# Kernel tuning notes

Measured on AMD Instinct MI355X. Metric: run time of the kernel, lower is better.

## Reference

```python
import jax, jax.numpy as jnp
import numpy as np

DN = ('NCHW', 'OIHW', 'NCHW')

def conv3x3(x, w):
    return jax.lax.conv_general_dilated(x, w, (1, 1), ((1, 1), (1, 1)), dimension_numbers=DN)

def dsc(x, w1, w2):
    # DynamicSparseConv: per-sample per-channel softmax 3x3 depthwise kernel + residual
    B, C, H, W = x.shape
    pooled = x.mean(axis=(2, 3))                                  # [B, C] (AdaptiveAvgPool2d(1))
    h = jax.nn.gelu(pooled @ w1.T, approximate=False)             # [B, Cr] (1x1 conv == matmul)
    logits = (h @ w2.T).reshape(B, C, 9)                          # [B, C, 9]
    wk = jax.nn.softmax(logits, axis=2)
    # 3x3 patches: [B, C*9, H, W], feature dim ordered (C, kh, kw)
    patches = jax.lax.conv_general_dilated_patches(x, (3, 3), (1, 1), ((1, 1), (1, 1)))
    patches = patches.reshape(B, C, 9, H, W)
    out = jnp.einsum('bckhw,bck->bchw', patches, wk)
    return out + x

def pixel_shuffle(x, r):
    B, C, H, W = x.shape
    c = C // (r * r)
    return x.reshape(B, c, r, r, H, W).transpose(0, 1, 4, 2, 5, 3).reshape(B, c, H * r, W * r)

def setup_inputs() -> dict:
    key = jax.random.key(0)
    ks = jax.random.split(key, 12)
    B, C, H, W, OUT = 16, 128, 64, 64, 64
    CR = max(4, C // 8)            # 16
    RE = max(4, OUT // 8)          # 8
    s = 0.05
    return {
        'x1': jax.random.normal(ks[0], (B, C, H, W), jnp.float32),
        'x2': jax.random.normal(ks[1], (B, C, H, W), jnp.float32),
        'd1_w1': jax.random.normal(ks[2], (CR, C), jnp.float32) * s,
        'd1_w2': jax.random.normal(ks[3], (9 * C, CR), jnp.float32) * s,
        'd2_w1': jax.random.normal(ks[4], (CR, C), jnp.float32) * s,
        'd2_w2': jax.random.normal(ks[5], (9 * C, CR), jnp.float32) * s,
        'align_w': jax.random.normal(ks[6], (C, 2 * C), jnp.float32) * s,
        'up_w1': jax.random.normal(ks[7], (4 * C, C, 3, 3), jnp.float32) * s,
        'up_w2': jax.random.normal(ks[8], (OUT, C), jnp.float32) * s,
        're_w1': jax.random.normal(ks[9], (RE, OUT, 3, 3), jnp.float32) * s,
        're_w2': jax.random.normal(ks[10], (OUT, RE, 3, 3), jnp.float32) * s,
    }

def reference(x1, x2, d1_w1, d1_w2, d2_w1, d2_w2, align_w, up_w1, up_w2, re_w1, re_w2):
    def dynamic_block(x):  # shared weights for both inputs (same nn.Sequential)
        x = dsc(x, d1_w1, d1_w2)
        x = jax.nn.relu(x)
        return dsc(x, d2_w1, d2_w2)
    a = dynamic_block(x1)
    b = dynamic_block(x2)
    fused = jnp.einsum('bchw,oc->bohw', jnp.concatenate([a, b], axis=1), align_w)  # 1x1 conv
    u = conv3x3(fused, up_w1)            # [B, 4C, H, W]
    u = pixel_shuffle(u, 2)              # [B, C, 2H, 2W]
    up = jnp.einsum('bchw,oc->bohw', u, up_w2)  # [B, OUT, 2H, 2W]
    re = conv3x3(jax.nn.relu(conv3x3(up, re_w1)), re_w2)
    return up + re
```

## Files before the change

### kernel.cpp

```cpp
#include <hip/hip_runtime.h>
#include <math.h>

typedef unsigned short ushort;
typedef short bf16x8 __attribute__((ext_vector_type(8)));
typedef ushort us8 __attribute__((ext_vector_type(8)));
typedef float f32x16 __attribute__((ext_vector_type(16)));
typedef float f32x4 __attribute__((ext_vector_type(4)));

static const size_t OFF_POOLED = 0;
static const size_t OFF_WK     = 4096;
static const size_t OFF_WT     = 40960;
static const size_t OFF_WF     = 188416;
static const size_t OFF_AW1    = 204800;
static const size_t OFF_AW2    = 209408;
static const size_t OFF_T      = 262144;
static const size_t OFF_AB     = 8650752;
static const size_t OFF_F      = 17039360;

static __device__ __forceinline__ ushort f2bf(float f) {
    unsigned int u = __builtin_bit_cast(unsigned int, f);
    u += 0x7FFF + ((u >> 16) & 1);
    return (ushort)(u >> 16);
}
static __device__ __forceinline__ float bf2f(ushort u) {
    return __builtin_bit_cast(float, ((unsigned int)u) << 16);
}

__global__ __launch_bounds__(256) void pool_both_kernel(const float* __restrict__ x1,
                                                        const float* __restrict__ x2,
                                                        float* __restrict__ pooled) {
    int bc = blockIdx.x;
    const float* x = (bc >> 11) ? x2 : x1;
    const float4* p = (const float4*)(x + (size_t)(bc & 2047) * 4096);
    float s = 0.f;
    for (int i = threadIdx.x; i < 1024; i += 256) {
        float4 v = p[i];
        s += v.x + v.y + v.z + v.w;
    }
    #pragma unroll
    for (int off = 32; off; off >>= 1) s += __shfl_down(s, off);
    __shared__ float r4[4];
    if ((threadIdx.x & 63) == 0) r4[threadIdx.x >> 6] = s;
    __syncthreads();
    if (threadIdx.x == 0) pooled[bc] = (r4[0] + r4[1] + r4[2] + r4[3]) * (1.f / 4096.f);
}

__global__ __launch_bounds__(128) void wk_kernel(const float* __restrict__ pooled,
                                                 const float* __restrict__ w1,
                                                 const float* __restrict__ w2,
                                                 float* __restrict__ wk) {
    int b = blockIdx.x;
    __shared__ float sp[128];
    __shared__ float sh[16];
    int t = threadIdx.x;
    sp[t] = pooled[b * 128 + t];
    __syncthreads();
    if (t < 16) {
        float acc = 0.f;
        #pragma unroll 4
        for (int c = 0; c < 128; c++) acc += w1[t * 128 + c] * sp[c];
        sh[t] = 0.5f * acc * (1.f + erff(acc * 0.70710678118654752f));
    }
    __syncthreads();
    float lg[9];
    float m = -INFINITY;
    #pragma unroll
    for (int k = 0; k < 9; k++) {
        float acc = 0.f;
        const float* wr = w2 + (size_t)(t * 9 + k) * 16;
        #pragma unroll
        for (int r = 0; r < 16; r++) acc += wr[r] * sh[r];
        lg[k] = acc;
        m = fmaxf(m, acc);
    }
    float se = 0.f;
    #pragma unroll
    for (int k = 0; k < 9; k++) { lg[k] = expf(lg[k] - m); se += lg[k]; }
    float inv = 1.f / se;
    #pragma unroll
    for (int k = 0; k < 9; k++) wk[(size_t)(b * 128 + t) * 9 + k] = lg[k] * inv;
}

__global__ __launch_bounds__(256) void dsc1_kernel(const float* __restrict__ x1,
                                                   const float* __restrict__ x2,
                                                   const float* __restrict__ wk,
                                                   ushort* __restrict__ y,
                                                   float* __restrict__ pooled2) {
    int bc = blockIdx.x;
    const float* xp = ((bc >> 11) ? x2 : x1) + (size_t)(bc & 2047) * 4096;
    ushort* yp = y + (size_t)bc * 4096;
    __shared__ float tile[66 * 66];
    __shared__ float r4[4];
    int t = threadIdx.x;
    for (int i = t; i < 66 * 66; i += 256) tile[i] = 0.f;
    __syncthreads();
    const float4* xp4 = (const float4*)xp;
    for (int i = t; i < 1024; i += 256) {
        float4 v = xp4[i];
        int h = i >> 4, w = (i & 15) * 4;
        float* d = &tile[(h + 1) * 66 + w + 1];
        d[0] = v.x; d[1] = v.y; d[2] = v.z; d[3] = v.w;
    }
    __syncthreads();
    float kk[9];
    #pragma unroll
    for (int k = 0; k < 9; k++) kk[k] = wk[(size_t)bc * 9 + k];
    float psum = 0.f;
    for (int i = t * 2; i < 4096; i += 512) {
        int h = i >> 6, w = i & 63;
        const float* c = &tile[h * 66 + w];
        float v0 = kk[0]*c[0] + kk[1]*c[1] + kk[2]*c[2]
                 + kk[3]*c[66] + kk[4]*c[67] + kk[5]*c[68]
                 + kk[6]*c[132] + kk[7]*c[133] + kk[8]*c[134] + c[67];
        float v1 = kk[0]*c[1] + kk[1]*c[2] + kk[2]*c[3]
                 + kk[3]*c[67] + kk[4]*c[68] + kk[5]*c[69]
                 + kk[6]*c[133] + kk[7]*c[134] + kk[8]*c[135] + c[68];
        v0 = fmaxf(v0, 0.f); v1 = fmaxf(v1, 0.f);
        psum += v0 + v1;
        ushort2 pk = {f2bf(v0), f2bf(v1)};
        *(ushort2*)&yp[i] = pk;
    }
    #pragma unroll
    for (int off = 32; off; off >>= 1) psum += __shfl_down(psum, off);
    if ((t & 63) == 0) r4[t >> 6] = psum;
    __syncthreads();
    if (t == 0) pooled2[bc] = (r4[0] + r4[1] + r4[2] + r4[3]) * (1.f / 4096.f);
}

__global__ __launch_bounds__(256) void dsc2_kernel(const ushort* __restrict__ x,
                                                   const float* __restrict__ wk,
                                                   ushort* __restrict__ y) {
    int bc = blockIdx.x;
    const ushort* xp = x + (size_t)bc * 4096;
    ushort* yp = y + (size_t)bc * 4096;
    __shared__ float tile[66 * 66];
    int t = threadIdx.x;
    for (int i = t; i < 66 * 66; i += 256) tile[i] = 0.f;
    __syncthreads();
    for (int i = t; i < 512; i += 256) {
        int4 raw = *(const int4*)&xp[i * 8];
        const ushort* u = (const ushort*)&raw;
        int h = i >> 3, w = (i & 7) * 8;
        float* d = &tile[(h + 1) * 66 + w + 1];
        #pragma unroll
        for (int j = 0; j < 8; j++) d[j] = bf2f(u[j]);
    }
    __syncthreads();
    float kk[9];
    #pragma unroll
    for (int k = 0; k < 9; k++) kk[k] = wk[(size_t)bc * 9 + k];
    for (int i = t * 2; i < 4096; i += 512) {
        int h = i >> 6, w = i & 63;
        const float* c = &tile[h * 66 + w];
        float v0 = kk[0]*c[0] + kk[1]*c[1] + kk[2]*c[2]
                 + kk[3]*c[66] + kk[4]*c[67] + kk[5]*c[68]
                 + kk[6]*c[132] + kk[7]*c[133] + kk[8]*c[134] + c[67];
        float v1 = kk[0]*c[1] + kk[1]*c[2] + kk[2]*c[3]
                 + kk[3]*c[67] + kk[4]*c[68] + kk[5]*c[69]
                 + kk[6]*c[133] + kk[7]*c[134] + kk[8]*c[135] + c[68];
        ushort2 pk = {f2bf(v0), f2bf(v1)};
        *(ushort2*)&yp[i] = pk;
    }
}

__global__ __launch_bounds__(256) void awprep_kernel(const float* __restrict__ W,
                                                     ushort* __restrict__ Wf) {
    int t = threadIdx.x;
    #pragma unroll 1
    for (int i = 0; i < 16; i++) {
        int tk = t + (i << 8);
        int step = tk >> 8, mt = (tk >> 6) & 3, lane = tk & 63;
        int o = mt * 32 + (lane & 31);
        int cb = step * 16 + (lane >> 5) * 8;
        #pragma unroll
        for (int j = 0; j < 8; j++) Wf[(size_t)tk * 8 + j] = f2bf(W[o * 256 + cb + j]);
    }
}

__global__ __launch_bounds__(256, 2) void align_mfma_kernel(const ushort* __restrict__ A,
                                                            const ushort* __restrict__ Bv,
                                                            const ushort* __restrict__ Wf,
                                                            ushort* __restrict__ F) {
    __shared__ ushort Xs[2 * 128 * 8];
    const int b = blockIdx.y;
    const int px0 = blockIdx.x << 7;
    const int tid = threadIdx.x;
    const int wave = tid >> 6, lane = tid & 63;
    const int l31 = lane & 31, half = lane >> 5;

    f32x16 acc[4];
    #pragma unroll
    for (int mt = 0; mt < 4; mt++)
        #pragma unroll
        for (int r = 0; r < 16; r++) acc[mt][r] = 0.f;

    const int cg0 = tid >> 7, pxs0 = tid & 127;
    const int bfofs = (wave * 32 + l31) * 8 + half * 1024;

    for (int step = 0; step < 16; step++) {
        const ushort* src =
            (step < 8 ? A : Bv) + (((size_t)(b * 128 + (step & 7) * 16)) << 12) + px0;
        if (step) __syncthreads();
        #pragma unroll
        for (int q = 0; q < 2; q++) {
            int cg = cg0 + q * 2, px = pxs0;
            ushort v0 = src[((size_t)(cg * 4 + 0) << 12) + px];
            ushort v1 = src[((size_t)(cg * 4 + 1) << 12) + px];
            ushort v2 = src[((size_t)(cg * 4 + 2) << 12) + px];
            ushort v3 = src[((size_t)(cg * 4 + 3) << 12) + px];
            ushort4 pk = {v0, v1, v2, v3};
            *(ushort4*)&Xs[(cg >> 1) * 1024 + px * 8 + (cg & 1) * 4] = pk;
        }
        __syncthreads();
        bf16x8 bfrag = *(const bf16x8*)&Xs[bfofs];
        const bf16x8* wf = (const bf16x8*)(Wf + ((size_t)step * 4 * 64 + lane) * 8);
        #pragma unroll
        for (int mt = 0; mt < 4; mt++)
            acc[mt] = __builtin_amdgcn_mfma_f32_32x32x16_bf16(wf[mt * 64], bfrag, acc[mt], 0, 0, 0);
    }
    ushort* fp = F + ((size_t)(b * 4096 + px0 + wave * 32 + l31)) * 128;
    #pragma unroll
    for (int mt = 0; mt < 4; mt++) {
        #pragma unroll
        for (int g = 0; g < 4; g++) {
            ushort4 pk = {f2bf(acc[mt][g * 4 + 0]), f2bf(acc[mt][g * 4 + 1]),
                          f2bf(acc[mt][g * 4 + 2]), f2bf(acc[mt][g * 4 + 3])};
            *(ushort4*)(fp + mt * 32 + half * 4 + 8 * g) = pk;
        }
    }
}

__global__ __launch_bounds__(256) void wcomb_kernel(const float* __restrict__ w1,
                                                    const float* __restrict__ w2,
                                                    ushort* __restrict__ Awt) {
    int idx = blockIdx.x * 256 + threadIdx.x;
    int j = idx & 7;
    int lane = (idx >> 3) & 63;
    int mt = (idx >> 9) & 3;
    int mh = (idx >> 11) & 1;
    int s = idx >> 12;
    int tap = s >> 3, c16 = s & 7;
    int arow = lane & 31;
    int o_sem = (mt & 1) * 32 + (arow & 3) + 4 * ((arow >> 3) & 3) + 16 * ((arow >> 2) & 1);
    int ph = 2 * mh + (mt >> 1);
    int cin = c16 * 16 + (lane >> 5) * 8 + j;
    float acc = 0.f;
    #pragma unroll 4
    for (int c = 0; c < 128; c++)
        acc += w2[o_sem * 128 + c] * w1[((size_t)(c * 4 + ph) * 128 + cin) * 9 + tap];
    Awt[idx] = f2bf(acc);
}

__global__ __launch_bounds__(256) void aw1prep_kernel(const float* __restrict__ w1,
                                                      ushort* __restrict__ Aw1) {
    int idx = blockIdx.x * 256 + threadIdx.x;
    if (idx >= 9216) return;
    int j = idx & 7, lane = (idx >> 3) & 63, s = idx >> 9;
    int m = lane & 15, kq = lane >> 4;
    int tap = s >> 1, ch = s & 1;
    int cin = ch * 32 + kq * 8 + j;
    float v = (m < 8) ? w1[((size_t)(m * 64 + cin)) * 9 + tap] : 0.f;
    Aw1[idx] = f2bf(v);
}

__global__ __launch_bounds__(256) void aw2prep_kernel(const float* __restrict__ w2,
                                                      ushort* __restrict__ Aw2) {
    int idx = blockIdx.x * 256 + threadIdx.x;
    if (idx >= 5120) return;
    int j = idx & 7, lane = (idx >> 3) & 63, mt = (idx >> 9) & 1, s = idx >> 10;
    int m = mt * 32 + (lane & 31), half = lane >> 5;
    int k = s * 16 + half * 8 + j;
    int tap = k >> 3, c = k & 7;
    float v = (tap < 9) ? w2[((size_t)(m * 8 + c)) * 9 + tap] : 0.f;
    Aw2[idx] = f2bf(v);
}

__global__ __launch_bounds__(256, 2) void up_mfma_kernel(const ushort* __restrict__ F,
                                                         const ushort* __restrict__ Awt,
                                                         ushort* __restrict__ U) {
    __shared__ ushort Xs[180 * 128];
    const int b = blockIdx.y;
    const int tr = blockIdx.x >> 3, tc = blockIdx.x & 7;
    const int tid = threadIdx.x;
    const int wave = tid >> 6, lane = tid & 63;
    const int l31 = lane & 31, half = lane >> 5;
    const int mh = wave >> 1, nh = wave & 1;

    for (int idx = tid; idx < 2880; idx += 256) {
        int px = idx >> 4, q = idx & 15;
        int r = px / 10, c = px - r * 10;
        int gh = tr * 16 - 1 + r, gw = tc * 8 - 1 + c;
        int4 v = {0, 0, 0, 0};
        if ((unsigned)gh < 64u && (unsigned)gw < 64u)
            v = *(const int4*)(F + ((size_t)(b * 4096 + gh * 64 + gw)) * 128 + q * 8);
        *(int4*)&Xs[px * 128 + ((q ^ (px & 7)) << 3)] = v;
    }
    __syncthreads();

    f32x16 acc[4][2];
    #pragma unroll
    for (int mt = 0; mt < 4; mt++)
        #pragma unroll
        for (int nt = 0; nt < 2; nt++)
            #pragma unroll
            for (int r = 0; r < 16; r++) acc[mt][nt][r] = 0.f;

    int xpos[2];
    #pragma unroll
    for (int nt = 0; nt < 2; nt++) {
        int pxl = nh * 64 + nt * 32 + l31;
        xpos[nt] = (pxl >> 3) * 10 + (pxl & 7);
    }

    const ushort* abase = Awt + (size_t)(mh * 4) * 512 + lane * 8;

    #define LDA(ss, mt) (*(const bf16x8*)(abase + (size_t)(ss) * 4096 + (mt) * 512))
    #define LDB(ss, nt) ({                                                   \
        int tap_ = (ss) >> 3, c16_ = (ss) & 7;                               \
        int ky_ = (tap_ * 11) >> 5;                      \
        int kx_ = tap_ - ky_ * 3;                                            \
        int p_ = xpos[nt] + ky_ * 10 + kx_;                                  \
        int qq_ = c16_ * 2 + half;                                           \
        *(const bf16x8*)&Xs[p_ * 128 + ((qq_ ^ (p_ & 7)) << 3)];             \
    })

    bf16x8 AS0[4], AS1[4], AS2[4], AS3[4], B0[2], B1[2];
    #pragma unroll
    for (int mt = 0; mt < 4; mt++) {
        AS0[mt] = LDA(0, mt);
        AS1[mt] = LDA(1, mt);
        AS2[mt] = LDA(2, mt);
        AS3[mt] = LDA(3, mt);
    }
    B0[0] = LDB(0, 0); B0[1] = LDB(0, 1);
    B1[0] = LDB(1, 0); B1[1] = LDB(1, 1);

    #define SUBSTEP(ASET, BSET, sa, sb)                                              \
    {                                                                                \
        _Pragma("unroll")                                                            \
        for (int mt = 0; mt < 4; mt++) {                                             \
            acc[mt][0] = __builtin_amdgcn_mfma_f32_32x32x16_bf16(ASET[mt], BSET[0], acc[mt][0], 0, 0, 0); \
            acc[mt][1] = __builtin_amdgcn_mfma_f32_32x32x16_bf16(ASET[mt], BSET[1], acc[mt][1], 0, 0, 0); \
        }                                                                            \
        _Pragma("unroll")                                                            \
        for (int mt = 0; mt < 4; mt++) ASET[mt] = LDA(sa, mt);                       \
        BSET[0] = LDB(sb, 0); BSET[1] = LDB(sb, 1);                                  \
    }

    #pragma unroll 1
    for (int s = 0; s < 72; s += 4) {
        int sa0 = (s + 4 < 72) ? s + 4 : 0;
        int sa1 = (s + 5 < 72) ? s + 5 : 0;
        int sa2 = (s + 6 < 72) ? s + 6 : 0;
        int sa3 = (s + 7 < 72) ? s + 7 : 0;
        int sb2 = (s + 4 < 72) ? s + 4 : 0;
        int sb3 = (s + 5 < 72) ? s + 5 : 0;
        SUBSTEP(AS0, B0, sa0, s + 2)
        SUBSTEP(AS1, B1, sa1, s + 3)
        SUBSTEP(AS2, B0, sa2, sb2)
        SUBSTEP(AS3, B1, sa3, sb3)
    }
    #undef SUBSTEP
    #undef LDA
    #undef LDB

    #pragma unroll
    for (int nt = 0; nt < 2; nt++) {
        int pxl = nh * 64 + nt * 32 + l31;
        int Y = 2 * (tr * 16 + (pxl >> 3)) + mh;
        int X = 2 * (tc * 8 + (pxl & 7));
        #pragma unroll
        for (int mt = 0; mt < 4; mt++) {
            ushort* up = U + ((size_t)((b * 128 + Y) * 128 + X + (mt >> 1))) * 64
                       + (mt & 1) * 32 + half * 16;
            us8 p0, p1;
            #pragma unroll
            for (int i = 0; i < 8; i++) {
                p0[i] = f2bf(acc[mt][nt][i]);
                p1[i] = f2bf(acc[mt][nt][8 + i]);
            }
            *(us8*)up = p0;
            *(us8*)(up + 8) = p1;
        }
    }
}

__global__ __launch_bounds__(256, 2) void re1_kernel(const ushort* __restrict__ U,
                                                     const ushort* __restrict__ Aw1,
                                                     ushort* __restrict__ R1) {
    __shared__ ushort Xs[324 * 72];
    __shared__ ushort As[18 * 64 * 8];
    const int b = blockIdx.y;
    const int ty = blockIdx.x >> 3, tx = blockIdx.x & 7;
    const int tid = threadIdx.x;
    const int wave = tid >> 6, lane = tid & 63;
    const int m16 = lane & 15, kq = lane >> 4;

    for (int idx = tid; idx < 1152; idx += 256)
        *(int4*)&As[idx * 8] = *(const int4*)(Aw1 + (size_t)idx * 8);
    for (int idx = tid; idx < 2592; idx += 256) {
        int px = idx >> 3, q = idx & 7;
        int r = px / 18, c = px - r * 18;
        int gY = ty * 16 - 1 + r, gX = tx * 16 - 1 + c;
        int4 v = {0, 0, 0, 0};
        if ((unsigned)gY < 128u && (unsigned)gX < 128u)
            v = *(const int4*)(U + ((size_t)((b * 128 + gY) * 128 + gX)) * 64 + q * 8);
        *(int4*)&Xs[px * 72 + q * 8] = v;
    }
    __syncthreads();

    f32x4 acc[4];
    #pragma unroll
    for (int nt = 0; nt < 4; nt++)
        #pragma unroll
        for (int r = 0; r < 4; r++) acc[nt][r] = 0.f;

    #pragma unroll 1
    for (int s = 0; s < 18; s++) {
        bf16x8 a = *(const bf16x8*)&As[(s * 64 + lane) * 8];
        int tap = s >> 1, ch = s & 1;
        int ky = tap / 3, kx = tap - ky * 3;
        int xo = (ky * 18 + kx) * 72 + ch * 32 + kq * 8;
        #pragma unroll
        for (int nt = 0; nt < 4; nt++) {
            int row = wave * 4 + nt;
            bf16x8 bv = *(const bf16x8*)&Xs[(row * 18 + m16) * 72 + xo];
            acc[nt] = __builtin_amdgcn_mfma_f32_16x16x32_bf16(a, bv, acc[nt], 0, 0, 0);
        }
    }
    if (kq < 2) {
        #pragma unroll
        for (int nt = 0; nt < 4; nt++) {
            int gY = ty * 16 + wave * 4 + nt, gX = tx * 16 + m16;
            ushort4 pk = {f2bf(fmaxf(acc[nt][0], 0.f)), f2bf(fmaxf(acc[nt][1], 0.f)),
                          f2bf(fmaxf(acc[nt][2], 0.f)), f2bf(fmaxf(acc[nt][3], 0.f))};
            *(ushort4*)(R1 + ((size_t)((b * 128 + gY) * 128 + gX)) * 8 + kq * 4) = pk;
        }
    }
}

__global__ __launch_bounds__(256, 2) void re2_kernel(const ushort* __restrict__ R1,
                                                     const ushort* __restrict__ U,
                                                     const ushort* __restrict__ Aw2,
                                                     float* __restrict__ out) {
    __shared__ ushort Xs[324 * 8];
    __shared__ ushort As[5 * 2 * 64 * 8];
    __shared__ ushort Us[256 * 68];
    const int b = blockIdx.y;
    const int ty = blockIdx.x >> 3, tx = blockIdx.x & 7;
    const int tid = threadIdx.x;
    const int wave = tid >> 6, lane = tid & 63;
    const int l31 = lane & 31, half = lane >> 5;

    for (int idx = tid; idx < 640; idx += 256)
        *(int4*)&As[idx * 8] = *(const int4*)(Aw2 + (size_t)idx * 8);
    for (int idx = tid; idx < 324; idx += 256) {
        int r = idx / 18, c = idx - r * 18;
        int gY = ty * 16 - 1 + r, gX = tx * 16 - 1 + c;
        int4 v = {0, 0, 0, 0};
        if ((unsigned)gY < 128u && (unsigned)gX < 128u)
            v = *(const int4*)(R1 + ((size_t)((b * 128 + gY) * 128 + gX)) * 8);
        *(int4*)&Xs[idx * 8] = v;
    }
    for (int idx = tid; idx < 2048; idx += 256) {
        int px = idx >> 3, q = idx & 7;
        int gY = ty * 16 + (px >> 4), gX = tx * 16 + (px & 15);
        const ushort* s = U + ((size_t)((b * 128 + gY) * 128 + gX)) * 64 + q * 8;
        ushort4 v0 = *(const ushort4*)s;
        ushort4 v1 = *(const ushort4*)(s + 4);
        *(ushort4*)&Us[px * 68 + q * 8] = v0;
        *(ushort4*)&Us[px * 68 + q * 8 + 4] = v1;
    }
    __syncthreads();

    f32x16 acc[2][2];
    #pragma unroll
    for (int mt = 0; mt < 2; mt++)
        #pragma unroll
        for (int nt = 0; nt < 2; nt++)
            #pragma unroll
            for (int r = 0; r < 16; r++) acc[mt][nt][r] = 0.f;

    #pragma unroll
    for (int s = 0; s < 5; s++) {
        bf16x8 a0 = *(const bf16x8*)&As[((s * 2 + 0) * 64 + lane) * 8];
        bf16x8 a1 = *(const bf16x8*)&As[((s * 2 + 1) * 64 + lane) * 8];
        int t = 2 * s + half;
        if (t > 8) t = 8;
        int ky = t / 3, kx = t - ky * 3;
        #pragma unroll
        for (int nt = 0; nt < 2; nt++) {
            int pxl = wave * 64 + nt * 32 + l31;
            int row = pxl >> 4, col = pxl & 15;
            bf16x8 bv = *(const bf16x8*)&Xs[((row + ky) * 18 + col + kx) * 8];
            acc[0][nt] = __builtin_amdgcn_mfma_f32_32x32x16_bf16(a0, bv, acc[0][nt], 0, 0, 0);
            acc[1][nt] = __builtin_amdgcn_mfma_f32_32x32x16_bf16(a1, bv, acc[1][nt], 0, 0, 0);
        }
    }
    #pragma unroll
    for (int mt = 0; mt < 2; mt++) {
        #pragma unroll
        for (int nt = 0; nt < 2; nt++) {
            int pxl = wave * 64 + nt * 32 + l31;
            int gY = ty * 16 + (pxl >> 4), gX = tx * 16 + (pxl & 15);
            #pragma unroll
            for (int r = 0; r < 16; r++) {
                int o = mt * 32 + (r & 3) + 8 * (r >> 2) + 4 * half;
                float v = acc[mt][nt][r] + bf2f(Us[pxl * 68 + o]);
                out[((size_t)(b * 64 + o) * 128 + gY) * 128 + gX] = v;
            }
        }
    }
}

extern "C" void kernel_launch(void* const* d_in, const int* in_sizes, int n_in,
                              void* d_out, int out_size, void* d_ws, size_t ws_size,
                              hipStream_t stream) {
    const float* x1      = (const float*)d_in[0];
    const float* x2      = (const float*)d_in[1];
    const float* d1_w1   = (const float*)d_in[2];
    const float* d1_w2   = (const float*)d_in[3];
    const float* d2_w1   = (const float*)d_in[4];
    const float* d2_w2   = (const float*)d_in[5];
    const float* align_w = (const float*)d_in[6];
    const float* up_w1   = (const float*)d_in[7];
    const float* up_w2   = (const float*)d_in[8];
    const float* re_w1   = (const float*)d_in[9];
    const float* re_w2   = (const float*)d_in[10];
    float* out = (float*)d_out;
    float* ws  = (float*)d_ws;

    float*  pooled = ws + OFF_POOLED;
    float*  wkb    = ws + OFF_WK;
    ushort* Awt    = (ushort*)(ws + OFF_WT);
    ushort* Wf     = (ushort*)(ws + OFF_WF);
    ushort* Aw1    = (ushort*)(ws + OFF_AW1);
    ushort* Aw2    = (ushort*)(ws + OFF_AW2);
    ushort* bufT   = (ushort*)(ws + OFF_T);
    ushort* R1     = (ushort*)(ws + OFF_T);
    ushort* bufAB  = (ushort*)(ws + OFF_AB);
    ushort* bufU   = (ushort*)(ws + OFF_AB);
    ushort* F      = (ushort*)(ws + OFF_F);

    wcomb_kernel<<<1152, 256, 0, stream>>>(up_w1, up_w2, Awt);
    awprep_kernel<<<1, 256, 0, stream>>>(align_w, Wf);
    aw1prep_kernel<<<36, 256, 0, stream>>>(re_w1, Aw1);
    aw2prep_kernel<<<20, 256, 0, stream>>>(re_w2, Aw2);

    pool_both_kernel<<<4096, 256, 0, stream>>>(x1, x2, pooled);
    wk_kernel<<<32, 128, 0, stream>>>(pooled, d1_w1, d1_w2, wkb);
    dsc1_kernel<<<4096, 256, 0, stream>>>(x1, x2, wkb, bufT, pooled);
    wk_kernel<<<32, 128, 0, stream>>>(pooled, d2_w1, d2_w2, wkb);
    dsc2_kernel<<<4096, 256, 0, stream>>>(bufT, wkb, bufAB);

    align_mfma_kernel<<<dim3(32, 16), 256, 0, stream>>>(bufAB, bufAB + 8388608, Wf, F);
    up_mfma_kernel<<<dim3(32, 16), 256, 0, stream>>>(F, Awt, bufU);
    re1_kernel<<<dim3(64, 16), 256, 0, stream>>>(bufU, Aw1, R1);
    re2_kernel<<<dim3(64, 16), 256, 0, stream>>>(R1, bufU, Aw2, out);
}
```

Measured before the change: 341.2 us.

## Stage up-conv weight tiles into LDS via async global_load_lds ring buffer

The up_mfma kernel used to load the A (weight) fragments for each K step directly from global memory into registers, with four register sets of prefetch. It now streams each 4096-element weight slice into a 4-slot LDS ring with global_load_lds, three steps ahead. Each step waits on vmcnt and a block barrier, then reads A and B fragments from LDS. MFMA bursts are wrapped in s_setprio so the math is prioritised. This cuts register pressure and duplicated global weight fetches across waves. The cost is 32KB of extra LDS, which may lower occupancy, plus a barrier on every step.

```diff
diff --git a/kernel.cpp b/kernel.cpp
--- a/kernel.cpp
+++ b/kernel.cpp
@@ -2,6 +2,7 @@
 #include <math.h>
 
 typedef unsigned short ushort;
+typedef unsigned int u32;
 typedef short bf16x8 __attribute__((ext_vector_type(8)));
 typedef ushort us8 __attribute__((ext_vector_type(8)));
 typedef float f32x16 __attribute__((ext_vector_type(16)));
@@ -279,12 +280,28 @@
                                                          const ushort* __restrict__ Awt,
                                                          ushort* __restrict__ U) {
     __shared__ ushort Xs[180 * 128];
+    __shared__ ushort Abuf[4 * 4096];
     const int b = blockIdx.y;
     const int tr = blockIdx.x >> 3, tc = blockIdx.x & 7;
     const int tid = threadIdx.x;
     const int wave = tid >> 6, lane = tid & 63;
     const int l31 = lane & 31, half = lane >> 5;
     const int mh = wave >> 1, nh = wave & 1;
+
+    #define STAGE_A(ss) do {                                                        \
+        int sb_ = (ss) & 3;                                                         \
+        const ushort* g0_ = Awt + (size_t)(ss) * 4096 + wave * 1024 + lane * 8;     \
+        __builtin_amdgcn_global_load_lds(                                           \
+            (const __attribute__((address_space(1))) u32*)g0_,                      \
+            (__attribute__((address_space(3))) u32*)&Abuf[sb_ * 4096 + wave * 1024],\
+            16, 0, 0);                                                              \
+        __builtin_amdgcn_global_load_lds(                                           \
+            (const __attribute__((address_space(1))) u32*)(g0_ + 512),              \
+            (__attribute__((address_space(3))) u32*)&Abuf[sb_ * 4096 + wave * 1024 + 512], \
+            16, 0, 0);                                                              \
+    } while (0)
+
+    STAGE_A(0); STAGE_A(1); STAGE_A(2);
 
     for (int idx = tid; idx < 2880; idx += 256) {
         int px = idx >> 4, q = idx & 15;
@@ -312,9 +329,7 @@
         xpos[nt] = (pxl >> 3) * 10 + (pxl & 7);
     }
 
-    const ushort* abase = Awt + (size_t)(mh * 4) * 512 + lane * 8;
-
-    #define LDA(ss, mt) (*(const bf16x8*)(abase + (size_t)(ss) * 4096 + (mt) * 512))
+    #define LDA(ss, mt) (*(const bf16x8*)&Abuf[((ss) & 3) * 4096 + (mh * 4 + (mt)) * 512 + lane * 8])
     #define LDB(ss, nt) ({                                                   \
         int tap_ = (ss) >> 3, c16_ = (ss) & 7;                               \
         int ky_ = (tap_ * 11) >> 5;                      \
@@ -324,45 +339,45 @@
         *(const bf16x8*)&Xs[p_ * 128 + ((qq_ ^ (p_ & 7)) << 3)];             \
     })
 
-    bf16x8 AS0[4], AS1[4], AS2[4], AS3[4], B0[2], B1[2];
-    #pragma unroll
-    for (int mt = 0; mt < 4; mt++) {
-        AS0[mt] = LDA(0, mt);
-        AS1[mt] = LDA(1, mt);
-        AS2[mt] = LDA(2, mt);
-        AS3[mt] = LDA(3, mt);
-    }
+    bf16x8 A0[4], A1[4], B0[2], B1[2];
+    #pragma unroll
+    for (int mt = 0; mt < 4; mt++) A0[mt] = LDA(0, mt);
     B0[0] = LDB(0, 0); B0[1] = LDB(0, 1);
-    B1[0] = LDB(1, 0); B1[1] = LDB(1, 1);
-
-    #define SUBSTEP(ASET, BSET, sa, sb)                                              \
-    {                                                                                \
+
+    #define MFMA8(ASET, BSET)                                                        \
+        __builtin_amdgcn_s_setprio(1);                                               \
         _Pragma("unroll")                                                            \
         for (int mt = 0; mt < 4; mt++) {                                             \
             acc[mt][0] = __builtin_amdgcn_mfma_f32_32x32x16_bf16(ASET[mt], BSET[0], acc[mt][0], 0, 0, 0); \
             acc[mt][1] = __builtin_amdgcn_mfma_f32_32x32x16_bf16(ASET[mt], BSET[1], acc[mt][1], 0, 0, 0); \
         }                                                                            \
+        __builtin_amdgcn_s_setprio(0);
+
+    #define HDR(VMC)                                                                 \
+        asm volatile("s_waitcnt vmcnt(" #VMC ")" ::: "memory");                      \
+        __builtin_amdgcn_s_barrier();                                                \
+        __builtin_amdgcn_sched_barrier(0);
+
+    #define RD(DST_A, DST_B, ss)                                                     \
         _Pragma("unroll")                                                            \
-        for (int mt = 0; mt < 4; mt++) ASET[mt] = LDA(sa, mt);                       \
-        BSET[0] = LDB(sb, 0); BSET[1] = LDB(sb, 1);                                  \
-    }
+        for (int mt = 0; mt < 4; mt++) DST_A[mt] = LDA(ss, mt);                      \
+        DST_B[0] = LDB(ss, 0); DST_B[1] = LDB(ss, 1);
 
     #pragma unroll 1
-    for (int s = 0; s < 72; s += 4) {
-        int sa0 = (s + 4 < 72) ? s + 4 : 0;
-        int sa1 = (s + 5 < 72) ? s + 5 : 0;
-        int sa2 = (s + 6 < 72) ? s + 6 : 0;
-        int sa3 = (s + 7 < 72) ? s + 7 : 0;
-        int sb2 = (s + 4 < 72) ? s + 4 : 0;
-        int sb3 = (s + 5 < 72) ? s + 5 : 0;
-        SUBSTEP(AS0, B0, sa0, s + 2)
-        SUBSTEP(AS1, B1, sa1, s + 3)
-        SUBSTEP(AS2, B0, sa2, sb2)
-        SUBSTEP(AS3, B1, sa3, sb3)
-    }
-    #undef SUBSTEP
+    for (int s = 0; s < 68; s += 2) {
+        HDR(2) STAGE_A(s + 3); RD(A1, B1, s + 1) MFMA8(A0, B0)
+        HDR(2) STAGE_A(s + 4); RD(A0, B0, s + 2) MFMA8(A1, B1)
+    }
+    HDR(2) STAGE_A(71); RD(A1, B1, 69) MFMA8(A0, B0)
+    HDR(2)              RD(A0, B0, 70) MFMA8(A1, B1)
+    HDR(0)              RD(A1, B1, 71) MFMA8(A0, B0)
+    MFMA8(A1, B1)
+    #undef HDR
+    #undef RD
+    #undef MFMA8
     #undef LDA
     #undef LDB
+    #undef STAGE_A
 
     #pragma unroll
     for (int nt = 0; nt < 2; nt++) {
```

New measurement: 351.3 us. +2.9%, slower.
